# Kernel optimization log

Measured on AMD Instinct MI355X. Metric: run time of the kernel, lower is better.

The kernel has to match this reference:

```python
import jax, jax.numpy as jnp
import numpy as np

N = 1024        # nodes
E = 524288      # directed edges
FE_IN, FE = 2, 64   # edge feat in / mid
FC = 128        # candidate (node) feat
L = 3           # EGAT conv layers
NEG_SLOPE = 0.2 # DGL leaky_relu default


def setup_inputs() -> dict:
    key = jax.random.key(0)
    ks = jax.random.split(key, 12)
    s = 0.05
    return {
        "node_feature": jax.random.normal(ks[0], (N, FC), jnp.float32),
        "edge_feature": jax.random.normal(ks[1], (E, FE_IN), jnp.float32),
        "src": jax.random.randint(ks[2], (E,), 0, N, dtype=jnp.int32),
        "dst": jax.random.randint(ks[3], (E,), 0, N, dtype=jnp.int32),
        # input edge linear (bias=True)
        "W_in": jax.random.normal(ks[4], (FE_IN, FE), jnp.float32) * s,
        "b_in": jnp.zeros((FE,), jnp.float32),
        # per-layer EGATConv params (num_heads=1)
        "W_ni": jax.random.normal(ks[5], (L, FC, FE), jnp.float32) * s,
        "W_nj": jax.random.normal(ks[6], (L, FC, FE), jnp.float32) * s,
        "W_fij": jax.random.normal(ks[7], (L, FE, FE), jnp.float32) * s,
        "W_node": jax.random.normal(ks[8], (L, FC, FC), jnp.float32) * s,
        "attn": jax.random.normal(ks[9], (L, FE), jnp.float32) * s,
        "bias_node": jnp.zeros((L, FC), jnp.float32),
    }


def _edge_softmax(e, dst):
    # softmax of edge logits e[E] over incoming edges of each dst node
    m = jax.ops.segment_max(e, dst, num_segments=N)
    ex = jnp.exp(e - m[dst])
    z = jax.ops.segment_sum(ex, dst, num_segments=N)
    return ex / z[dst]


def reference(node_feature, edge_feature, src, dst, W_in, b_in,
              W_ni, W_nj, W_fij, W_node, attn, bias_node):
    node = node_feature                       # [N, FC]
    ef = edge_feature @ W_in + b_in           # [E, FE]
    for l in range(L):
        f_ni = node @ W_ni[l]                 # [N, FE]
        f_nj = node @ W_nj[l]                 # [N, FE]
        # edge messages: gather src/dst projections + edge projection
        f_out = jax.nn.leaky_relu(f_ni[src] + f_nj[dst] + ef @ W_fij[l],
                                  NEG_SLOPE)  # [E, FE]
        e = jnp.einsum('ef,f->e', f_out, attn[l])   # [E]
        a = _edge_softmax(e, dst)                    # [E]
        h = node @ W_node[l] + bias_node[l]          # [N, FC]
        new_node = jax.ops.segment_sum(a[:, None] * h[src], dst,
                                       num_segments=N)  # [N, FC]
        # residual fusion (use_residual=True, num_heads=1 so squeeze is a no-op)
        node = node + new_node
        ef = ef + f_out
    return node
```

## Files before the change

kernel.cpp:

```cpp
#include <hip/hip_runtime.h>

#define N_NODES 1024
#define E_EDGES 524288
#define FE 64
#define FC 128
#define NLAYERS 3

typedef unsigned short u16;
typedef unsigned int u32;
typedef __attribute__((ext_vector_type(8))) short bf16x8;
typedef __attribute__((ext_vector_type(4))) float f32x4;
typedef __attribute__((ext_vector_type(8))) unsigned short u16x8;
typedef __attribute__((ext_vector_type(4))) unsigned int u32x4;

__device__ __forceinline__ float bf2f(u16 u) {
    return __uint_as_float(((u32)u) << 16);
}
__device__ __forceinline__ u32 cvt2bf(float lo, float hi) {
    u32 r;
    asm("v_cvt_pk_bf16_f32 %0, %1, %2" : "=v"(r) : "v"(lo), "v"(hi));
    return r;
}
__device__ __forceinline__ u16 f2bf(float f) {
    return (u16)cvt2bf(f, 0.f);
}

__global__ __launch_bounds__(256) void setup_kernel(
    const float* __restrict__ node_feature, const float* __restrict__ Wfij,
    u16* __restrict__ Wt,
    const float* __restrict__ Wni, const float* __restrict__ Wnj,
    const float* __restrict__ Wnode, const float* __restrict__ bias,
    u16* __restrict__ fni, u16* __restrict__ fnj,
    float* __restrict__ h, float* __restrict__ S, float* __restrict__ nodeA)
{
    __shared__ float row[FC];
    const int d = blockIdx.x;
    const int t = threadIdx.x;

    reinterpret_cast<float4*>(S + (size_t)d * N_NODES)[t] = make_float4(0.f, 0.f, 0.f, 0.f);

    if (t < FC) {
        const float v = node_feature[d * FC + t];
        nodeA[d * FC + t] = v;
        row[t] = v;
    }
    if (d < (NLAYERS * FE * FE) / 256) {
        const int i = d * 256 + t;
        const int l = i >> 12, rem = i & 4095;
        const int n = rem >> 6, k = rem & 63;
        Wt[(u32)(l * 4096 + n * 64 + k)] = f2bf(Wfij[(u32)(l * 4096 + k * 64 + n)]);
    }
    __syncthreads();

    if (t < 64) {
        float a0 = 0.f, a1 = 0.f;
        #pragma unroll 8
        for (int k = 0; k < FC; k += 2) {
            a0 = fmaf(row[k],     Wni[k * FE + t], a0);
            a1 = fmaf(row[k + 1], Wni[(k + 1) * FE + t], a1);
        }
        fni[d * FE + t] = f2bf(a0 + a1);
    } else if (t < 128) {
        const int f = t - 64;
        float a0 = 0.f, a1 = 0.f;
        #pragma unroll 8
        for (int k = 0; k < FC; k += 2) {
            a0 = fmaf(row[k],     Wnj[k * FE + f], a0);
            a1 = fmaf(row[k + 1], Wnj[(k + 1) * FE + f], a1);
        }
        fnj[d * FE + f] = f2bf(a0 + a1);
    } else {
        const int c = t - 128;
        float a0 = bias[c], a1 = 0.f;
        #pragma unroll 8
        for (int k = 0; k < FC; k += 2) {
            a0 = fmaf(row[k],     Wnode[k * FC + c], a0);
            a1 = fmaf(row[k + 1], Wnode[(k + 1) * FC + c], a1);
        }
        h[d * FC + c] = a0 + a1;
    }
}

template <bool FIRST, bool WRITE_EF>
__global__ void edge_mfma_kernel(
    u16* __restrict__ ef,
    const float* __restrict__ x,
    const float* __restrict__ Win,
    const float* __restrict__ bin,
    const u16* __restrict__ Wt,
    const u16* __restrict__ fni, const u16* __restrict__ fnj,
    const int* __restrict__ src, const int* __restrict__ dst,
    const float* __restrict__ attn,
    float* __restrict__ S)
{
    __shared__ __align__(16) u16 stage[4][16][72];
    __shared__ __align__(16) u16 fol[WRITE_EF ? 4 : 1][16][72];

    const int lane = threadIdx.x & 63;
    const int wid  = threadIdx.x >> 6;
    const int l15  = lane & 15;
    const int grp  = lane >> 4;
    const int wbase = blockIdx.x * 64 + wid * 16;

    #pragma unroll
    for (int it = 0; it < 2; it++) {
        const int row = it * 8 + (lane >> 3);
        const int e = wbase + row;
        const int c8 = (lane & 7) * 8;
        const u16x8 a = *reinterpret_cast<const u16x8*>(fni + (u32)(src[e] * FE + c8));
        const u16x8 b = *reinterpret_cast<const u16x8*>(fnj + (u32)(dst[e] * FE + c8));
        u32x4 s;
        #pragma unroll
        for (int j = 0; j < 4; j++) {
            s[j] = cvt2bf(bf2f(a[2*j]) + bf2f(b[2*j]),
                          bf2f(a[2*j+1]) + bf2f(b[2*j+1]));
        }
        *reinterpret_cast<u32x4*>(&stage[wid][row][c8]) = s;
    }

    bf16x8 afr0, afr1;
    if constexpr (FIRST) {
        const float2 xx = *reinterpret_cast<const float2*>(x + 2 * (u32)(wbase + l15));
        #pragma unroll
        for (int half = 0; half < 2; half++) {
            const int c0 = half * 32 + grp * 8;
            const float4 wA0 = *reinterpret_cast<const float4*>(Win + c0);
            const float4 wA1 = *reinterpret_cast<const float4*>(Win + c0 + 4);
            const float4 wB0 = *reinterpret_cast<const float4*>(Win + FE + c0);
            const float4 wB1 = *reinterpret_cast<const float4*>(Win + FE + c0 + 4);
            const float4 b0  = *reinterpret_cast<const float4*>(bin + c0);
            const float4 b1  = *reinterpret_cast<const float4*>(bin + c0 + 4);
            u32x4 fr;
            fr[0] = cvt2bf(fmaf(xx.x, wA0.x, fmaf(xx.y, wB0.x, b0.x)),
                           fmaf(xx.x, wA0.y, fmaf(xx.y, wB0.y, b0.y)));
            fr[1] = cvt2bf(fmaf(xx.x, wA0.z, fmaf(xx.y, wB0.z, b0.z)),
                           fmaf(xx.x, wA0.w, fmaf(xx.y, wB0.w, b0.w)));
            fr[2] = cvt2bf(fmaf(xx.x, wA1.x, fmaf(xx.y, wB1.x, b1.x)),
                           fmaf(xx.x, wA1.y, fmaf(xx.y, wB1.y, b1.y)));
            fr[3] = cvt2bf(fmaf(xx.x, wA1.z, fmaf(xx.y, wB1.z, b1.z)),
                           fmaf(xx.x, wA1.w, fmaf(xx.y, wB1.w, b1.w)));
            if (half == 0) afr0 = (bf16x8)fr; else afr1 = (bf16x8)fr;
        }
    } else {
        const u32 arow = (u32)(wbase + l15) * FE;
        afr0 = *reinterpret_cast<const bf16x8*>(ef + arow + grp * 8);
        afr1 = *reinterpret_cast<const bf16x8*>(ef + arow + 32 + grp * 8);
    }

    bf16x8 bfr[2][4];
    #pragma unroll
    for (int ks = 0; ks < 2; ks++)
        #pragma unroll
        for (int nt = 0; nt < 4; nt++)
            bfr[ks][nt] = *reinterpret_cast<const bf16x8*>(
                Wt + (u32)((nt * 16 + l15) * 64 + ks * 32 + grp * 8));

    f32x4 acc[4];
    #pragma unroll
    for (int nt = 0; nt < 4; nt++) {
        acc[nt] = (f32x4){0.f, 0.f, 0.f, 0.f};
        acc[nt] = __builtin_amdgcn_mfma_f32_16x16x32_bf16(afr0, bfr[0][nt], acc[nt], 0, 0, 0);
        acc[nt] = __builtin_amdgcn_mfma_f32_16x16x32_bf16(afr1, bfr[1][nt], acc[nt], 0, 0, 0);
    }

    float an[4];
    #pragma unroll
    for (int nt = 0; nt < 4; nt++) an[nt] = attn[nt * 16 + l15] * 1.44269504088896f;

    __builtin_amdgcn_wave_barrier();

    float logit[4] = {0.f, 0.f, 0.f, 0.f};
    #pragma unroll
    for (int nt = 0; nt < 4; nt++) {
        const int n = nt * 16 + l15;
        #pragma unroll
        for (int r = 0; r < 4; r++) {
            const int row = grp * 4 + r;
            float v = acc[nt][r] + bf2f(stage[wid][row][n]);
            v = fmaxf(v, 0.2f * v);
            logit[r] = fmaf(v, an[nt], logit[r]);
            if constexpr (WRITE_EF) fol[wid][row][n] = f2bf(v);
        }
    }

    #pragma unroll
    for (int r = 0; r < 4; r++) {
        float t = logit[r];
        t += __shfl_xor(t, 1, 16);
        t += __shfl_xor(t, 2, 16);
        t += __shfl_xor(t, 4, 16);
        t += __shfl_xor(t, 8, 16);
        if (l15 == 0) {
            const int e = wbase + grp * 4 + r;
            atomicAdd(S + (u32)(dst[e] * N_NODES + src[e]), exp2f(t));
        }
    }

    if constexpr (WRITE_EF) {
        __builtin_amdgcn_wave_barrier();
        const u16x8 fo0 = *reinterpret_cast<const u16x8*>(&fol[wid][l15][grp * 8]);
        const u16x8 fo1 = *reinterpret_cast<const u16x8*>(&fol[wid][l15][32 + grp * 8]);
        u32x4 o0, o1;
        #pragma unroll
        for (int j = 0; j < 4; j++) {
            o0[j] = cvt2bf(bf2f((u16)afr0[2*j])   + bf2f(fo0[2*j]),
                           bf2f((u16)afr0[2*j+1]) + bf2f(fo0[2*j+1]));
            o1[j] = cvt2bf(bf2f((u16)afr1[2*j])   + bf2f(fo1[2*j]),
                           bf2f((u16)afr1[2*j+1]) + bf2f(fo1[2*j+1]));
        }
        u16* gp = ef + (u32)(wbase + l15) * FE;
        *reinterpret_cast<u32x4*>(gp + grp * 8) = o0;
        *reinterpret_cast<u32x4*>(gp + 32 + grp * 8) = o1;
    }
}

template <bool LAST>
__global__ __launch_bounds__(256) void spmm_kernel(
    float* __restrict__ S, const float* __restrict__ h,
    const float* __restrict__ nin, float* __restrict__ nout,
    const float* __restrict__ Wni, const float* __restrict__ Wnj,
    const float* __restrict__ Wnode, const float* __restrict__ bias,
    u16* __restrict__ fni, u16* __restrict__ fnj, float* __restrict__ hnext)
{
    __shared__ float red[256];
    __shared__ float rs[2];
    __shared__ float row[FC];
    const int d = blockIdx.x;
    const int t = threadIdx.x;
    const int c = t & 127;
    const int half = t >> 7;
    const float* Srow = S + (size_t)d * N_NODES + half * 512;
    const float* hp = h + (size_t)half * 512 * FC;
    float a0 = 0.f, a1 = 0.f, a2 = 0.f, a3 = 0.f;
    float r0 = 0.f, r1 = 0.f, r2 = 0.f, r3 = 0.f;
    #pragma unroll 4
    for (int n = 0; n < 512; n += 4) {
        const float s0 = Srow[n], s1 = Srow[n+1], s2 = Srow[n+2], s3 = Srow[n+3];
        r0 += s0; r1 += s1; r2 += s2; r3 += s3;
        a0 = fmaf(s0, hp[n * FC + c], a0);
        a1 = fmaf(s1, hp[(n+1) * FC + c], a1);
        a2 = fmaf(s2, hp[(n+2) * FC + c], a2);
        a3 = fmaf(s3, hp[(n+3) * FC + c], a3);
    }
    red[t] = (a0 + a1) + (a2 + a3);
    if (c == 0) rs[half] = (r0 + r1) + (r2 + r3);
    __syncthreads();

    if constexpr (!LAST) {
        reinterpret_cast<float4*>(S + (size_t)d * N_NODES)[t] = make_float4(0.f, 0.f, 0.f, 0.f);
    }
    if (half == 0) {
        const float v = nin[d * FC + c] + (red[c] + red[128 + c]) / (rs[0] + rs[1]);
        nout[d * FC + c] = v;
        if constexpr (!LAST) row[c] = v;
    }

    if constexpr (!LAST) {
        __syncthreads();
        if (t < 64) {
            float b0 = 0.f, b1 = 0.f;
            #pragma unroll 8
            for (int k = 0; k < FC; k += 2) {
                b0 = fmaf(row[k],     Wni[k * FE + t], b0);
                b1 = fmaf(row[k + 1], Wni[(k + 1) * FE + t], b1);
            }
            fni[d * FE + t] = f2bf(b0 + b1);
        } else if (t < 128) {
            const int f = t - 64;
            float b0 = 0.f, b1 = 0.f;
            #pragma unroll 8
            for (int k = 0; k < FC; k += 2) {
                b0 = fmaf(row[k],     Wnj[k * FE + f], b0);
                b1 = fmaf(row[k + 1], Wnj[(k + 1) * FE + f], b1);
            }
            fnj[d * FE + f] = f2bf(b0 + b1);
        } else {
            const int cc = t - 128;
            float b0 = bias[cc], b1 = 0.f;
            #pragma unroll 8
            for (int k = 0; k < FC; k += 2) {
                b0 = fmaf(row[k],     Wnode[k * FC + cc], b0);
                b1 = fmaf(row[k + 1], Wnode[(k + 1) * FC + cc], b1);
            }
            hnext[d * FC + cc] = b0 + b1;
        }
    }
}

extern "C" void kernel_launch(void* const* d_in, const int* in_sizes, int n_in,
                              void* d_out, int out_size, void* d_ws, size_t ws_size,
                              hipStream_t stream)
{
    const float* node_feature = (const float*)d_in[0];
    const float* edge_feature = (const float*)d_in[1];
    const int*   src          = (const int*)d_in[2];
    const int*   dst          = (const int*)d_in[3];
    const float* W_in         = (const float*)d_in[4];
    const float* b_in         = (const float*)d_in[5];
    const float* W_ni         = (const float*)d_in[6];
    const float* W_nj         = (const float*)d_in[7];
    const float* W_fij        = (const float*)d_in[8];
    const float* W_node       = (const float*)d_in[9];
    const float* attn         = (const float*)d_in[10];
    const float* bias_node    = (const float*)d_in[11];
    float* out = (float*)d_out;

    char* ws = (char*)d_ws;
    size_t off = 0;
    auto alloc = [&](size_t bytes) -> void* {
        void* pp = ws + off;
        off += (bytes + 255) & ~(size_t)255;
        return pp;
    };
    u16*   ef    = (u16*)alloc((size_t)E_EDGES * FE * sizeof(u16));
    u16*   fni   = (u16*)alloc(N_NODES * FE * sizeof(u16));
    u16*   fnj   = (u16*)alloc(N_NODES * FE * sizeof(u16));
    float* h0    = (float*)alloc(N_NODES * FC * sizeof(float));
    float* h1    = (float*)alloc(N_NODES * FC * sizeof(float));
    float* S     = (float*)alloc((size_t)N_NODES * N_NODES * sizeof(float));
    float* nodeA = (float*)alloc(N_NODES * FC * sizeof(float));
    u16*   Wt    = (u16*)alloc((size_t)NLAYERS * FE * FE * sizeof(u16));
    float* hbuf[2] = {h0, h1};

    setup_kernel<<<N_NODES, 256, 0, stream>>>(
        node_feature, W_fij, Wt, W_ni, W_nj, W_node, bias_node,
        fni, fnj, h0, S, nodeA);

    for (int l = 0; l < NLAYERS; l++) {
        float* hl = hbuf[l & 1];
        float* hn = hbuf[(l + 1) & 1];

        if (l == 0) {
            edge_mfma_kernel<true, true><<<E_EDGES / 64, 256, 0, stream>>>(
                ef, edge_feature, W_in, b_in, Wt + (size_t)l * FE * FE,
                fni, fnj, src, dst, attn + (size_t)l * FE, S);
        } else if (l == NLAYERS - 1) {
            edge_mfma_kernel<false, false><<<E_EDGES / 64, 256, 0, stream>>>(
                ef, nullptr, nullptr, nullptr, Wt + (size_t)l * FE * FE,
                fni, fnj, src, dst, attn + (size_t)l * FE, S);
        } else {
            edge_mfma_kernel<false, true><<<E_EDGES / 64, 256, 0, stream>>>(
                ef, nullptr, nullptr, nullptr, Wt + (size_t)l * FE * FE,
                fni, fnj, src, dst, attn + (size_t)l * FE, S);
        }

        if (l == NLAYERS - 1) {
            spmm_kernel<true><<<N_NODES, 256, 0, stream>>>(
                S, hl, nodeA, out,
                nullptr, nullptr, nullptr, nullptr, nullptr, nullptr, nullptr);
        } else {
            const int ln = l + 1;
            spmm_kernel<false><<<N_NODES, 256, 0, stream>>>(
                S, hl, nodeA, nodeA,
                W_ni + (size_t)ln * FC * FE, W_nj + (size_t)ln * FC * FE,
                W_node + (size_t)ln * FC * FC, bias_node + (size_t)ln * FC,
                fni, fnj, hn);
        }
    }
}
```

Measured before the change: 280.0 us.

## Process two edge tiles per wave and four destination rows per spmm block

The edge kernel now handles 128 edges per block, with each wave doing two 16-edge tiles. All src/dst indices and fni/fnj gathers are issued up front, and indices are broadcast with shuffles instead of reloaded. The spmm kernel computes four destination rows per block, so each h load is reused across four S rows, and the row sums come from a separate vectorized pass. The aim is more memory-level parallelism and less redundant h traffic, at the cost of higher register pressure and fewer blocks.

```diff
diff --git a/kernel.cpp b/kernel.cpp
--- a/kernel.cpp
+++ b/kernel.cpp
@@ -100,51 +100,60 @@
     const int wid  = threadIdx.x >> 6;
     const int l15  = lane & 15;
     const int grp  = lane >> 4;
-    const int wbase = blockIdx.x * 64 + wid * 16;
-
-    #pragma unroll
-    for (int it = 0; it < 2; it++) {
-        const int row = it * 8 + (lane >> 3);
-        const int e = wbase + row;
-        const int c8 = (lane & 7) * 8;
-        const u16x8 a = *reinterpret_cast<const u16x8*>(fni + (u32)(src[e] * FE + c8));
-        const u16x8 b = *reinterpret_cast<const u16x8*>(fnj + (u32)(dst[e] * FE + c8));
-        u32x4 s;
-        #pragma unroll
-        for (int j = 0; j < 4; j++) {
-            s[j] = cvt2bf(bf2f(a[2*j]) + bf2f(b[2*j]),
-                          bf2f(a[2*j+1]) + bf2f(b[2*j+1]));
-        }
-        *reinterpret_cast<u32x4*>(&stage[wid][row][c8]) = s;
-    }
-
-    bf16x8 afr0, afr1;
-    if constexpr (FIRST) {
-        const float2 xx = *reinterpret_cast<const float2*>(x + 2 * (u32)(wbase + l15));
-        #pragma unroll
-        for (int half = 0; half < 2; half++) {
-            const int c0 = half * 32 + grp * 8;
-            const float4 wA0 = *reinterpret_cast<const float4*>(Win + c0);
-            const float4 wA1 = *reinterpret_cast<const float4*>(Win + c0 + 4);
-            const float4 wB0 = *reinterpret_cast<const float4*>(Win + FE + c0);
-            const float4 wB1 = *reinterpret_cast<const float4*>(Win + FE + c0 + 4);
-            const float4 b0  = *reinterpret_cast<const float4*>(bin + c0);
-            const float4 b1  = *reinterpret_cast<const float4*>(bin + c0 + 4);
-            u32x4 fr;
-            fr[0] = cvt2bf(fmaf(xx.x, wA0.x, fmaf(xx.y, wB0.x, b0.x)),
-                           fmaf(xx.x, wA0.y, fmaf(xx.y, wB0.y, b0.y)));
-            fr[1] = cvt2bf(fmaf(xx.x, wA0.z, fmaf(xx.y, wB0.z, b0.z)),
-                           fmaf(xx.x, wA0.w, fmaf(xx.y, wB0.w, b0.w)));
-            fr[2] = cvt2bf(fmaf(xx.x, wA1.x, fmaf(xx.y, wB1.x, b1.x)),
-                           fmaf(xx.x, wA1.y, fmaf(xx.y, wB1.y, b1.y)));
-            fr[3] = cvt2bf(fmaf(xx.x, wA1.z, fmaf(xx.y, wB1.z, b1.z)),
-                           fmaf(xx.x, wA1.w, fmaf(xx.y, wB1.w, b1.w)));
-            if (half == 0) afr0 = (bf16x8)fr; else afr1 = (bf16x8)fr;
-        }
-    } else {
-        const u32 arow = (u32)(wbase + l15) * FE;
-        afr0 = *reinterpret_cast<const bf16x8*>(ef + arow + grp * 8);
-        afr1 = *reinterpret_cast<const bf16x8*>(ef + arow + 32 + grp * 8);
+    const int block0 = blockIdx.x * 128;
+
+    int tb[2], sv[2], dv[2];
+    #pragma unroll
+    for (int tt = 0; tt < 2; tt++) {
+        tb[tt] = block0 + tt * 64 + wid * 16;
+        sv[tt] = src[tb[tt] + l15];
+        dv[tt] = dst[tb[tt] + l15];
+    }
+
+    u16x8 ga[2][2], gb[2][2];
+    #pragma unroll
+    for (int tt = 0; tt < 2; tt++) {
+        #pragma unroll
+        for (int it = 0; it < 2; it++) {
+            const int row = it * 8 + (lane >> 3);
+            const int c8 = (lane & 7) * 8;
+            const int s = __shfl(sv[tt], row, 16);
+            const int d = __shfl(dv[tt], row, 16);
+            ga[tt][it] = *reinterpret_cast<const u16x8*>(fni + (u32)(s * FE + c8));
+            gb[tt][it] = *reinterpret_cast<const u16x8*>(fnj + (u32)(d * FE + c8));
+        }
+    }
+
+    bf16x8 afr[2][2];
+    #pragma unroll
+    for (int tt = 0; tt < 2; tt++) {
+        if constexpr (FIRST) {
+            const float2 xx = *reinterpret_cast<const float2*>(x + 2 * (u32)(tb[tt] + l15));
+            #pragma unroll
+            for (int half = 0; half < 2; half++) {
+                const int c0 = half * 32 + grp * 8;
+                const float4 wA0 = *reinterpret_cast<const float4*>(Win + c0);
+                const float4 wA1 = *reinterpret_cast<const float4*>(Win + c0 + 4);
+                const float4 wB0 = *reinterpret_cast<const float4*>(Win + FE + c0);
+                const float4 wB1 = *reinterpret_cast<const float4*>(Win + FE + c0 + 4);
+                const float4 b0  = *reinterpret_cast<const float4*>(bin + c0);
+                const float4 b1  = *reinterpret_cast<const float4*>(bin + c0 + 4);
+                u32x4 fr;
+                fr[0] = cvt2bf(fmaf(xx.x, wA0.x, fmaf(xx.y, wB0.x, b0.x)),
+                               fmaf(xx.x, wA0.y, fmaf(xx.y, wB0.y, b0.y)));
+                fr[1] = cvt2bf(fmaf(xx.x, wA0.z, fmaf(xx.y, wB0.z, b0.z)),
+                               fmaf(xx.x, wA0.w, fmaf(xx.y, wB0.w, b0.w)));
+                fr[2] = cvt2bf(fmaf(xx.x, wA1.x, fmaf(xx.y, wB1.x, b1.x)),
+                               fmaf(xx.x, wA1.y, fmaf(xx.y, wB1.y, b1.y)));
+                fr[3] = cvt2bf(fmaf(xx.x, wA1.z, fmaf(xx.y, wB1.z, b1.z)),
+                               fmaf(xx.x, wA1.w, fmaf(xx.y, wB1.w, b1.w)));
+                afr[tt][half] = (bf16x8)fr;
+            }
+        } else {
+            const u32 arow = (u32)(tb[tt] + l15) * FE;
+            afr[tt][0] = *reinterpret_cast<const bf16x8*>(ef + arow + grp * 8);
+            afr[tt][1] = *reinterpret_cast<const bf16x8*>(ef + arow + 32 + grp * 8);
+        }
     }
 
     bf16x8 bfr[2][4];
@@ -155,62 +164,81 @@
             bfr[ks][nt] = *reinterpret_cast<const bf16x8*>(
                 Wt + (u32)((nt * 16 + l15) * 64 + ks * 32 + grp * 8));
 
-    f32x4 acc[4];
-    #pragma unroll
-    for (int nt = 0; nt < 4; nt++) {
-        acc[nt] = (f32x4){0.f, 0.f, 0.f, 0.f};
-        acc[nt] = __builtin_amdgcn_mfma_f32_16x16x32_bf16(afr0, bfr[0][nt], acc[nt], 0, 0, 0);
-        acc[nt] = __builtin_amdgcn_mfma_f32_16x16x32_bf16(afr1, bfr[1][nt], acc[nt], 0, 0, 0);
-    }
-
     float an[4];
     #pragma unroll
     for (int nt = 0; nt < 4; nt++) an[nt] = attn[nt * 16 + l15] * 1.44269504088896f;
 
-    __builtin_amdgcn_wave_barrier();
-
-    float logit[4] = {0.f, 0.f, 0.f, 0.f};
-    #pragma unroll
-    for (int nt = 0; nt < 4; nt++) {
-        const int n = nt * 16 + l15;
+    #pragma unroll
+    for (int tt = 0; tt < 2; tt++) {
+        #pragma unroll
+        for (int it = 0; it < 2; it++) {
+            const int row = it * 8 + (lane >> 3);
+            const int c8 = (lane & 7) * 8;
+            u32x4 s;
+            #pragma unroll
+            for (int j = 0; j < 4; j++) {
+                s[j] = cvt2bf(bf2f(ga[tt][it][2*j])   + bf2f(gb[tt][it][2*j]),
+                              bf2f(ga[tt][it][2*j+1]) + bf2f(gb[tt][it][2*j+1]));
+            }
+            *reinterpret_cast<u32x4*>(&stage[wid][row][c8]) = s;
+        }
+
+        f32x4 acc[4];
+        #pragma unroll
+        for (int nt = 0; nt < 4; nt++) {
+            acc[nt] = (f32x4){0.f, 0.f, 0.f, 0.f};
+            acc[nt] = __builtin_amdgcn_mfma_f32_16x16x32_bf16(afr[tt][0], bfr[0][nt], acc[nt], 0, 0, 0);
+            acc[nt] = __builtin_amdgcn_mfma_f32_16x16x32_bf16(afr[tt][1], bfr[1][nt], acc[nt], 0, 0, 0);
+        }
+
+        __builtin_amdgcn_wave_barrier();
+
+        float logit[4] = {0.f, 0.f, 0.f, 0.f};
+        #pragma unroll
+        for (int nt = 0; nt < 4; nt++) {
+            const int n = nt * 16 + l15;
+            #pragma unroll
+            for (int r = 0; r < 4; r++) {
+                const int row = grp * 4 + r;
+                float v = acc[nt][r] + bf2f(stage[wid][row][n]);
+                v = fmaxf(v, 0.2f * v);
+                logit[r] = fmaf(v, an[nt], logit[r]);
+                if constexpr (WRITE_EF) fol[wid][row][n] = f2bf(v);
+            }
+        }
+
         #pragma unroll
         for (int r = 0; r < 4; r++) {
-            const int row = grp * 4 + r;
-            float v = acc[nt][r] + bf2f(stage[wid][row][n]);
-            v = fmaxf(v, 0.2f * v);
-            logit[r] = fmaf(v, an[nt], logit[r]);
-            if constexpr (WRITE_EF) fol[wid][row][n] = f2bf(v);
-        }
-    }
-
-    #pragma unroll
-    for (int r = 0; r < 4; r++) {
-        float t = logit[r];
-        t += __shfl_xor(t, 1, 16);
-        t += __shfl_xor(t, 2, 16);
-        t += __shfl_xor(t, 4, 16);
-        t += __shfl_xor(t, 8, 16);
-        if (l15 == 0) {
-            const int e = wbase + grp * 4 + r;
-            atomicAdd(S + (u32)(dst[e] * N_NODES + src[e]), exp2f(t));
-        }
-    }
-
-    if constexpr (WRITE_EF) {
+            float t = logit[r];
+            t += __shfl_xor(t, 1, 16);
+            t += __shfl_xor(t, 2, 16);
+            t += __shfl_xor(t, 4, 16);
+            t += __shfl_xor(t, 8, 16);
+            const int sidx = __shfl(sv[tt], grp * 4 + r, 16);
+            const int didx = __shfl(dv[tt], grp * 4 + r, 16);
+            if (l15 == 0) {
+                atomicAdd(S + (u32)(didx * N_NODES + sidx), exp2f(t));
+            }
+        }
+
+        if constexpr (WRITE_EF) {
+            __builtin_amdgcn_wave_barrier();
+            const u16x8 fo0 = *reinterpret_cast<const u16x8*>(&fol[wid][l15][grp * 8]);
+            const u16x8 fo1 = *reinterpret_cast<const u16x8*>(&fol[wid][l15][32 + grp * 8]);
+            u32x4 o0, o1;
+            #pragma unroll
+            for (int j = 0; j < 4; j++) {
+                o0[j] = cvt2bf(bf2f((u16)afr[tt][0][2*j])   + bf2f(fo0[2*j]),
+                               bf2f((u16)afr[tt][0][2*j+1]) + bf2f(fo0[2*j+1]));
+                o1[j] = cvt2bf(bf2f((u16)afr[tt][1][2*j])   + bf2f(fo1[2*j]),
+                               bf2f((u16)afr[tt][1][2*j+1]) + bf2f(fo1[2*j+1]));
+            }
+            u16* gp = ef + (u32)(tb[tt] + l15) * FE;
+            *reinterpret_cast<u32x4*>(gp + grp * 8) = o0;
+            *reinterpret_cast<u32x4*>(gp + 32 + grp * 8) = o1;
+        }
+
         __builtin_amdgcn_wave_barrier();
-        const u16x8 fo0 = *reinterpret_cast<const u16x8*>(&fol[wid][l15][grp * 8]);
-        const u16x8 fo1 = *reinterpret_cast<const u16x8*>(&fol[wid][l15][32 + grp * 8]);
-        u32x4 o0, o1;
-        #pragma unroll
-        for (int j = 0; j < 4; j++) {
-            o0[j] = cvt2bf(bf2f((u16)afr0[2*j])   + bf2f(fo0[2*j]),
-                           bf2f((u16)afr0[2*j+1]) + bf2f(fo0[2*j+1]));
-            o1[j] = cvt2bf(bf2f((u16)afr1[2*j])   + bf2f(fo1[2*j]),
-                           bf2f((u16)afr1[2*j+1]) + bf2f(fo1[2*j+1]));
-        }
-        u16* gp = ef + (u32)(wbase + l15) * FE;
-        *reinterpret_cast<u32x4*>(gp + grp * 8) = o0;
-        *reinterpret_cast<u32x4*>(gp + 32 + grp * 8) = o1;
     }
 }
 
@@ -222,67 +250,100 @@
     const float* __restrict__ Wnode, const float* __restrict__ bias,
     u16* __restrict__ fni, u16* __restrict__ fnj, float* __restrict__ hnext)
 {
-    __shared__ float red[256];
-    __shared__ float rs[2];
-    __shared__ float row[FC];
-    const int d = blockIdx.x;
+    __shared__ float red[2][128][4];
+    __shared__ float rs[4];
+    __shared__ float row[4][FC];
+    const int d0 = blockIdx.x * 4;
     const int t = threadIdx.x;
     const int c = t & 127;
     const int half = t >> 7;
-    const float* Srow = S + (size_t)d * N_NODES + half * 512;
-    const float* hp = h + (size_t)half * 512 * FC;
+
+    const float* hp = h + (u32)(half * 512 * FC) + c;
+    const u32 sbase = (u32)(d0 * N_NODES) + half * 512;
     float a0 = 0.f, a1 = 0.f, a2 = 0.f, a3 = 0.f;
-    float r0 = 0.f, r1 = 0.f, r2 = 0.f, r3 = 0.f;
     #pragma unroll 4
-    for (int n = 0; n < 512; n += 4) {
-        const float s0 = Srow[n], s1 = Srow[n+1], s2 = Srow[n+2], s3 = Srow[n+3];
-        r0 += s0; r1 += s1; r2 += s2; r3 += s3;
-        a0 = fmaf(s0, hp[n * FC + c], a0);
-        a1 = fmaf(s1, hp[(n+1) * FC + c], a1);
-        a2 = fmaf(s2, hp[(n+2) * FC + c], a2);
-        a3 = fmaf(s3, hp[(n+3) * FC + c], a3);
-    }
-    red[t] = (a0 + a1) + (a2 + a3);
-    if (c == 0) rs[half] = (r0 + r1) + (r2 + r3);
+    for (int n = 0; n < 512; n++) {
+        const float hv = hp[(u32)n * FC];
+        const float s0 = S[sbase + n];
+        const float s1 = S[sbase + N_NODES + n];
+        const float s2 = S[sbase + 2 * N_NODES + n];
+        const float s3 = S[sbase + 3 * N_NODES + n];
+        a0 = fmaf(s0, hv, a0);
+        a1 = fmaf(s1, hv, a1);
+        a2 = fmaf(s2, hv, a2);
+        a3 = fmaf(s3, hv, a3);
+    }
+    red[half][c][0] = a0; red[half][c][1] = a1;
+    red[half][c][2] = a2; red[half][c][3] = a3;
+
+    {
+        const int w = t >> 6, wl = t & 63;
+        const float4* sr = reinterpret_cast<const float4*>(S + (u32)(d0 + w) * N_NODES);
+        float rsv = 0.f;
+        #pragma unroll
+        for (int q = 0; q < 4; q++) {
+            const float4 v = sr[wl + 64 * q];
+            rsv += (v.x + v.y) + (v.z + v.w);
+        }
+        rsv += __shfl_xor(rsv, 1);  rsv += __shfl_xor(rsv, 2);
+        rsv += __shfl_xor(rsv, 4);  rsv += __shfl_xor(rsv, 8);
+        rsv += __shfl_xor(rsv, 16); rsv += __shfl_xor(rsv, 32);
+        if (wl == 0) rs[w] = rsv;
+    }
     __syncthreads();
 
     if constexpr (!LAST) {
-        reinterpret_cast<float4*>(S + (size_t)d * N_NODES)[t] = make_float4(0.f, 0.f, 0.f, 0.f);
-    }
-    if (half == 0) {
-        const float v = nin[d * FC + c] + (red[c] + red[128 + c]) / (rs[0] + rs[1]);
-        nout[d * FC + c] = v;
-        if constexpr (!LAST) row[c] = v;
+        float4* sz = reinterpret_cast<float4*>(S + (u32)d0 * N_NODES);
+        #pragma unroll
+        for (int q = 0; q < 4; q++) sz[t + 256 * q] = make_float4(0.f, 0.f, 0.f, 0.f);
+    }
+    if (t < 128) {
+        #pragma unroll
+        for (int r = 0; r < 4; r++) {
+            const float v = nin[(u32)(d0 + r) * FC + t]
+                          + (red[0][t][r] + red[1][t][r]) / rs[r];
+            nout[(u32)(d0 + r) * FC + t] = v;
+            if constexpr (!LAST) row[r][t] = v;
+        }
     }
 
     if constexpr (!LAST) {
         __syncthreads();
         if (t < 64) {
-            float b0 = 0.f, b1 = 0.f;
-            #pragma unroll 8
-            for (int k = 0; k < FC; k += 2) {
-                b0 = fmaf(row[k],     Wni[k * FE + t], b0);
-                b1 = fmaf(row[k + 1], Wni[(k + 1) * FE + t], b1);
-            }
-            fni[d * FE + t] = f2bf(b0 + b1);
+            #pragma unroll
+            for (int r = 0; r < 4; r++) {
+                float b0 = 0.f, b1 = 0.f;
+                #pragma unroll 8
+                for (int k = 0; k < FC; k += 2) {
+                    b0 = fmaf(row[r][k],     Wni[k * FE + t], b0);
+                    b1 = fmaf(row[r][k + 1], Wni[(k + 1) * FE + t], b1);
+                }
+                fni[(u32)(d0 + r) * FE + t] = f2bf(b0 + b1);
+            }
         } else if (t < 128) {
             const int f = t - 64;
-            float b0 = 0.f, b1 = 0.f;
-            #pragma unroll 8
-            for (int k = 0; k < FC; k += 2) {
-                b0 = fmaf(row[k],     Wnj[k * FE + f], b0);
-                b1 = fmaf(row[k + 1], Wnj[(k + 1) * FE + f], b1);
-            }
-            fnj[d * FE + f] = f2bf(b0 + b1);
+            #pragma unroll
+            for (int r = 0; r < 4; r++) {
+                float b0 = 0.f, b1 = 0.f;
+                #pragma unroll 8
+                for (int k = 0; k < FC; k += 2) {
+                    b0 = fmaf(row[r][k],     Wnj[k * FE + f], b0);
+                    b1 = fmaf(row[r][k + 1], Wnj[(k + 1) * FE + f], b1);
+                }
+                fnj[(u32)(d0 + r) * FE + f] = f2bf(b0 + b1);
+            }
         } else {
             const int cc = t - 128;
-            float b0 = bias[cc], b1 = 0.f;
-            #pragma unroll 8
-            for (int k = 0; k < FC; k += 2) {
-                b0 = fmaf(row[k],     Wnode[k * FC + cc], b0);
-                b1 = fmaf(row[k + 1], Wnode[(k + 1) * FC + cc], b1);
-            }
-            hnext[d * FC + cc] = b0 + b1;
+            #pragma unroll
+            for (int r = 0; r < 4; r++) {
+                float b0 = bias[cc], b1 = 0.f;
+                #pragma unroll 8
+                for (int k = 0; k < FC; k += 2) {
+                    b0 = fmaf(row[r][k],     Wnode[k * FC + cc], b0);
+                    b1 = fmaf(row[r][k + 1], Wnode[(k + 1) * FC + cc], b1);
+                }
+                hnext[(u32)(d0 + r) * FC + cc] = b0 + b1;
+            }
         }
     }
 }
@@ -331,26 +392,26 @@
         float* hn = hbuf[(l + 1) & 1];
 
         if (l == 0) {
-            edge_mfma_kernel<true, true><<<E_EDGES / 64, 256, 0, stream>>>(
+            edge_mfma_kernel<true, true><<<E_EDGES / 128, 256, 0, stream>>>(
                 ef, edge_feature, W_in, b_in, Wt + (size_t)l * FE * FE,
                 fni, fnj, src, dst, attn + (size_t)l * FE, S);
         } else if (l == NLAYERS - 1) {
-            edge_mfma_kernel<false, false><<<E_EDGES / 64, 256, 0, stream>>>(
+            edge_mfma_kernel<false, false><<<E_EDGES / 128, 256, 0, stream>>>(
                 ef, nullptr, nullptr, nullptr, Wt + (size_t)l * FE * FE,
                 fni, fnj, src, dst, attn + (size_t)l * FE, S);
         } else {
-            edge_mfma_kernel<false, true><<<E_EDGES / 64, 256, 0, stream>>>(
+            edge_mfma_kernel<false, true><<<E_EDGES / 128, 256, 0, stream>>>(
                 ef, nullptr, nullptr, nullptr, Wt + (size_t)l * FE * FE,
                 fni, fnj, src, dst, attn + (size_t)l * FE, S);
         }
 
         if (l == NLAYERS - 1) {
-            spmm_kernel<true><<<N_NODES, 256, 0, stream>>>(
+            spmm_kernel<true><<<N_NODES / 4, 256, 0, stream>>>(
                 S, hl, nodeA, out,
                 nullptr, nullptr, nullptr, nullptr, nullptr, nullptr, nullptr);
         } else {
             const int ln = l + 1;
-            spmm_kernel<false><<<N_NODES, 256, 0, stream>>>(
+            spmm_kernel<false><<<N_NODES / 4, 256, 0, stream>>>(
                 S, hl, nodeA, nodeA,
                 W_ni + (size_t)ln * FC * FE, W_nj + (size_t)ln * FC * FE,
                 W_node + (size_t)ln * FC * FC, bias_node + (size_t)ln * FC,
```

New measurement: 272.1 us. 2.8% less time.

## Process two edge tiles per wave with early batched gathers and shuffled indices

Applied to the files above, without the earlier changes.

Each wave now handles two 16-edge tiles per block, halving the grid. It loads src/dst once per lane and broadcasts them with shuffles instead of re-reading them. All fni/fnj gathers and ef loads for both tiles are issued up front, so more memory requests are in flight before the MFMA and epilogue work. This also amortizes the weight-fragment and attention loads over twice as many edges, at the cost of higher register pressure and fewer blocks. Some 64-bit index math in the spmm kernel is narrowed to 32-bit.

```diff
diff --git a/kernel.cpp b/kernel.cpp
--- a/kernel.cpp
+++ b/kernel.cpp
@@ -100,51 +100,60 @@
     const int wid  = threadIdx.x >> 6;
     const int l15  = lane & 15;
     const int grp  = lane >> 4;
-    const int wbase = blockIdx.x * 64 + wid * 16;
-
-    #pragma unroll
-    for (int it = 0; it < 2; it++) {
-        const int row = it * 8 + (lane >> 3);
-        const int e = wbase + row;
-        const int c8 = (lane & 7) * 8;
-        const u16x8 a = *reinterpret_cast<const u16x8*>(fni + (u32)(src[e] * FE + c8));
-        const u16x8 b = *reinterpret_cast<const u16x8*>(fnj + (u32)(dst[e] * FE + c8));
-        u32x4 s;
-        #pragma unroll
-        for (int j = 0; j < 4; j++) {
-            s[j] = cvt2bf(bf2f(a[2*j]) + bf2f(b[2*j]),
-                          bf2f(a[2*j+1]) + bf2f(b[2*j+1]));
-        }
-        *reinterpret_cast<u32x4*>(&stage[wid][row][c8]) = s;
-    }
-
-    bf16x8 afr0, afr1;
-    if constexpr (FIRST) {
-        const float2 xx = *reinterpret_cast<const float2*>(x + 2 * (u32)(wbase + l15));
-        #pragma unroll
-        for (int half = 0; half < 2; half++) {
-            const int c0 = half * 32 + grp * 8;
-            const float4 wA0 = *reinterpret_cast<const float4*>(Win + c0);
-            const float4 wA1 = *reinterpret_cast<const float4*>(Win + c0 + 4);
-            const float4 wB0 = *reinterpret_cast<const float4*>(Win + FE + c0);
-            const float4 wB1 = *reinterpret_cast<const float4*>(Win + FE + c0 + 4);
-            const float4 b0  = *reinterpret_cast<const float4*>(bin + c0);
-            const float4 b1  = *reinterpret_cast<const float4*>(bin + c0 + 4);
-            u32x4 fr;
-            fr[0] = cvt2bf(fmaf(xx.x, wA0.x, fmaf(xx.y, wB0.x, b0.x)),
-                           fmaf(xx.x, wA0.y, fmaf(xx.y, wB0.y, b0.y)));
-            fr[1] = cvt2bf(fmaf(xx.x, wA0.z, fmaf(xx.y, wB0.z, b0.z)),
-                           fmaf(xx.x, wA0.w, fmaf(xx.y, wB0.w, b0.w)));
-            fr[2] = cvt2bf(fmaf(xx.x, wA1.x, fmaf(xx.y, wB1.x, b1.x)),
-                           fmaf(xx.x, wA1.y, fmaf(xx.y, wB1.y, b1.y)));
-            fr[3] = cvt2bf(fmaf(xx.x, wA1.z, fmaf(xx.y, wB1.z, b1.z)),
-                           fmaf(xx.x, wA1.w, fmaf(xx.y, wB1.w, b1.w)));
-            if (half == 0) afr0 = (bf16x8)fr; else afr1 = (bf16x8)fr;
-        }
-    } else {
-        const u32 arow = (u32)(wbase + l15) * FE;
-        afr0 = *reinterpret_cast<const bf16x8*>(ef + arow + grp * 8);
-        afr1 = *reinterpret_cast<const bf16x8*>(ef + arow + 32 + grp * 8);
+    const int block0 = blockIdx.x * 128;
+
+    int tb[2], sv[2], dv[2];
+    #pragma unroll
+    for (int tt = 0; tt < 2; tt++) {
+        tb[tt] = block0 + tt * 64 + wid * 16;
+        sv[tt] = src[tb[tt] + l15];
+        dv[tt] = dst[tb[tt] + l15];
+    }
+
+    u16x8 ga[2][2], gb[2][2];
+    #pragma unroll
+    for (int tt = 0; tt < 2; tt++) {
+        #pragma unroll
+        for (int it = 0; it < 2; it++) {
+            const int row = it * 8 + (lane >> 3);
+            const int c8 = (lane & 7) * 8;
+            const int s = __shfl(sv[tt], row, 16);
+            const int d = __shfl(dv[tt], row, 16);
+            ga[tt][it] = *reinterpret_cast<const u16x8*>(fni + (u32)(s * FE + c8));
+            gb[tt][it] = *reinterpret_cast<const u16x8*>(fnj + (u32)(d * FE + c8));
+        }
+    }
+
+    bf16x8 afr[2][2];
+    #pragma unroll
+    for (int tt = 0; tt < 2; tt++) {
+        if constexpr (FIRST) {
+            const float2 xx = *reinterpret_cast<const float2*>(x + 2 * (u32)(tb[tt] + l15));
+            #pragma unroll
+            for (int half = 0; half < 2; half++) {
+                const int c0 = half * 32 + grp * 8;
+                const float4 wA0 = *reinterpret_cast<const float4*>(Win + c0);
+                const float4 wA1 = *reinterpret_cast<const float4*>(Win + c0 + 4);
+                const float4 wB0 = *reinterpret_cast<const float4*>(Win + FE + c0);
+                const float4 wB1 = *reinterpret_cast<const float4*>(Win + FE + c0 + 4);
+                const float4 b0  = *reinterpret_cast<const float4*>(bin + c0);
+                const float4 b1  = *reinterpret_cast<const float4*>(bin + c0 + 4);
+                u32x4 fr;
+                fr[0] = cvt2bf(fmaf(xx.x, wA0.x, fmaf(xx.y, wB0.x, b0.x)),
+                               fmaf(xx.x, wA0.y, fmaf(xx.y, wB0.y, b0.y)));
+                fr[1] = cvt2bf(fmaf(xx.x, wA0.z, fmaf(xx.y, wB0.z, b0.z)),
+                               fmaf(xx.x, wA0.w, fmaf(xx.y, wB0.w, b0.w)));
+                fr[2] = cvt2bf(fmaf(xx.x, wA1.x, fmaf(xx.y, wB1.x, b1.x)),
+                               fmaf(xx.x, wA1.y, fmaf(xx.y, wB1.y, b1.y)));
+                fr[3] = cvt2bf(fmaf(xx.x, wA1.z, fmaf(xx.y, wB1.z, b1.z)),
+                               fmaf(xx.x, wA1.w, fmaf(xx.y, wB1.w, b1.w)));
+                afr[tt][half] = (bf16x8)fr;
+            }
+        } else {
+            const u32 arow = (u32)(tb[tt] + l15) * FE;
+            afr[tt][0] = *reinterpret_cast<const bf16x8*>(ef + arow + grp * 8);
+            afr[tt][1] = *reinterpret_cast<const bf16x8*>(ef + arow + 32 + grp * 8);
+        }
     }
 
     bf16x8 bfr[2][4];
@@ -155,62 +164,81 @@
             bfr[ks][nt] = *reinterpret_cast<const bf16x8*>(
                 Wt + (u32)((nt * 16 + l15) * 64 + ks * 32 + grp * 8));
 
-    f32x4 acc[4];
-    #pragma unroll
-    for (int nt = 0; nt < 4; nt++) {
-        acc[nt] = (f32x4){0.f, 0.f, 0.f, 0.f};
-        acc[nt] = __builtin_amdgcn_mfma_f32_16x16x32_bf16(afr0, bfr[0][nt], acc[nt], 0, 0, 0);
-        acc[nt] = __builtin_amdgcn_mfma_f32_16x16x32_bf16(afr1, bfr[1][nt], acc[nt], 0, 0, 0);
-    }
-
     float an[4];
     #pragma unroll
     for (int nt = 0; nt < 4; nt++) an[nt] = attn[nt * 16 + l15] * 1.44269504088896f;
 
-    __builtin_amdgcn_wave_barrier();
-
-    float logit[4] = {0.f, 0.f, 0.f, 0.f};
-    #pragma unroll
-    for (int nt = 0; nt < 4; nt++) {
-        const int n = nt * 16 + l15;
+    #pragma unroll
+    for (int tt = 0; tt < 2; tt++) {
+        #pragma unroll
+        for (int it = 0; it < 2; it++) {
+            const int row = it * 8 + (lane >> 3);
+            const int c8 = (lane & 7) * 8;
+            u32x4 s;
+            #pragma unroll
+            for (int j = 0; j < 4; j++) {
+                s[j] = cvt2bf(bf2f(ga[tt][it][2*j])   + bf2f(gb[tt][it][2*j]),
+                              bf2f(ga[tt][it][2*j+1]) + bf2f(gb[tt][it][2*j+1]));
+            }
+            *reinterpret_cast<u32x4*>(&stage[wid][row][c8]) = s;
+        }
+
+        f32x4 acc[4];
+        #pragma unroll
+        for (int nt = 0; nt < 4; nt++) {
+            acc[nt] = (f32x4){0.f, 0.f, 0.f, 0.f};
+            acc[nt] = __builtin_amdgcn_mfma_f32_16x16x32_bf16(afr[tt][0], bfr[0][nt], acc[nt], 0, 0, 0);
+            acc[nt] = __builtin_amdgcn_mfma_f32_16x16x32_bf16(afr[tt][1], bfr[1][nt], acc[nt], 0, 0, 0);
+        }
+
+        __builtin_amdgcn_wave_barrier();
+
+        float logit[4] = {0.f, 0.f, 0.f, 0.f};
+        #pragma unroll
+        for (int nt = 0; nt < 4; nt++) {
+            const int n = nt * 16 + l15;
+            #pragma unroll
+            for (int r = 0; r < 4; r++) {
+                const int row = grp * 4 + r;
+                float v = acc[nt][r] + bf2f(stage[wid][row][n]);
+                v = fmaxf(v, 0.2f * v);
+                logit[r] = fmaf(v, an[nt], logit[r]);
+                if constexpr (WRITE_EF) fol[wid][row][n] = f2bf(v);
+            }
+        }
+
         #pragma unroll
         for (int r = 0; r < 4; r++) {
-            const int row = grp * 4 + r;
-            float v = acc[nt][r] + bf2f(stage[wid][row][n]);
-            v = fmaxf(v, 0.2f * v);
-            logit[r] = fmaf(v, an[nt], logit[r]);
-            if constexpr (WRITE_EF) fol[wid][row][n] = f2bf(v);
-        }
-    }
-
-    #pragma unroll
-    for (int r = 0; r < 4; r++) {
-        float t = logit[r];
-        t += __shfl_xor(t, 1, 16);
-        t += __shfl_xor(t, 2, 16);
-        t += __shfl_xor(t, 4, 16);
-        t += __shfl_xor(t, 8, 16);
-        if (l15 == 0) {
-            const int e = wbase + grp * 4 + r;
-            atomicAdd(S + (u32)(dst[e] * N_NODES + src[e]), exp2f(t));
-        }
-    }
-
-    if constexpr (WRITE_EF) {
+            float t = logit[r];
+            t += __shfl_xor(t, 1, 16);
+            t += __shfl_xor(t, 2, 16);
+            t += __shfl_xor(t, 4, 16);
+            t += __shfl_xor(t, 8, 16);
+            const int sidx = __shfl(sv[tt], grp * 4 + r, 16);
+            const int didx = __shfl(dv[tt], grp * 4 + r, 16);
+            if (l15 == 0) {
+                atomicAdd(S + (u32)(didx * N_NODES + sidx), exp2f(t));
+            }
+        }
+
+        if constexpr (WRITE_EF) {
+            __builtin_amdgcn_wave_barrier();
+            const u16x8 fo0 = *reinterpret_cast<const u16x8*>(&fol[wid][l15][grp * 8]);
+            const u16x8 fo1 = *reinterpret_cast<const u16x8*>(&fol[wid][l15][32 + grp * 8]);
+            u32x4 o0, o1;
+            #pragma unroll
+            for (int j = 0; j < 4; j++) {
+                o0[j] = cvt2bf(bf2f((u16)afr[tt][0][2*j])   + bf2f(fo0[2*j]),
+                               bf2f((u16)afr[tt][0][2*j+1]) + bf2f(fo0[2*j+1]));
+                o1[j] = cvt2bf(bf2f((u16)afr[tt][1][2*j])   + bf2f(fo1[2*j]),
+                               bf2f((u16)afr[tt][1][2*j+1]) + bf2f(fo1[2*j+1]));
+            }
+            u16* gp = ef + (u32)(tb[tt] + l15) * FE;
+            *reinterpret_cast<u32x4*>(gp + grp * 8) = o0;
+            *reinterpret_cast<u32x4*>(gp + 32 + grp * 8) = o1;
+        }
+
         __builtin_amdgcn_wave_barrier();
-        const u16x8 fo0 = *reinterpret_cast<const u16x8*>(&fol[wid][l15][grp * 8]);
-        const u16x8 fo1 = *reinterpret_cast<const u16x8*>(&fol[wid][l15][32 + grp * 8]);
-        u32x4 o0, o1;
-        #pragma unroll
-        for (int j = 0; j < 4; j++) {
-            o0[j] = cvt2bf(bf2f((u16)afr0[2*j])   + bf2f(fo0[2*j]),
-                           bf2f((u16)afr0[2*j+1]) + bf2f(fo0[2*j+1]));
-            o1[j] = cvt2bf(bf2f((u16)afr1[2*j])   + bf2f(fo1[2*j]),
-                           bf2f((u16)afr1[2*j+1]) + bf2f(fo1[2*j+1]));
-        }
-        u16* gp = ef + (u32)(wbase + l15) * FE;
-        *reinterpret_cast<u32x4*>(gp + grp * 8) = o0;
-        *reinterpret_cast<u32x4*>(gp + 32 + grp * 8) = o1;
     }
 }
 
@@ -229,8 +257,8 @@
     const int t = threadIdx.x;
     const int c = t & 127;
     const int half = t >> 7;
-    const float* Srow = S + (size_t)d * N_NODES + half * 512;
-    const float* hp = h + (size_t)half * 512 * FC;
+    const float* Srow = S + (u32)d * N_NODES + half * 512;
+    const float* hp = h + (u32)(half * 512 * FC);
     float a0 = 0.f, a1 = 0.f, a2 = 0.f, a3 = 0.f;
     float r0 = 0.f, r1 = 0.f, r2 = 0.f, r3 = 0.f;
     #pragma unroll 4
@@ -247,7 +275,7 @@
     __syncthreads();
 
     if constexpr (!LAST) {
-        reinterpret_cast<float4*>(S + (size_t)d * N_NODES)[t] = make_float4(0.f, 0.f, 0.f, 0.f);
+        reinterpret_cast<float4*>(S + (u32)d * N_NODES)[t] = make_float4(0.f, 0.f, 0.f, 0.f);
     }
     if (half == 0) {
         const float v = nin[d * FC + c] + (red[c] + red[128 + c]) / (rs[0] + rs[1]);
@@ -331,15 +359,15 @@
         float* hn = hbuf[(l + 1) & 1];
 
         if (l == 0) {
-            edge_mfma_kernel<true, true><<<E_EDGES / 64, 256, 0, stream>>>(
+            edge_mfma_kernel<true, true><<<E_EDGES / 128, 256, 0, stream>>>(
                 ef, edge_feature, W_in, b_in, Wt + (size_t)l * FE * FE,
                 fni, fnj, src, dst, attn + (size_t)l * FE, S);
         } else if (l == NLAYERS - 1) {
-            edge_mfma_kernel<false, false><<<E_EDGES / 64, 256, 0, stream>>>(
+            edge_mfma_kernel<false, false><<<E_EDGES / 128, 256, 0, stream>>>(
                 ef, nullptr, nullptr, nullptr, Wt + (size_t)l * FE * FE,
                 fni, fnj, src, dst, attn + (size_t)l * FE, S);
         } else {
-            edge_mfma_kernel<false, true><<<E_EDGES / 64, 256, 0, stream>>>(
+            edge_mfma_kernel<false, true><<<E_EDGES / 128, 256, 0, stream>>>(
                 ef, nullptr, nullptr, nullptr, Wt + (size_t)l * FE * FE,
                 fni, fnj, src, dst, attn + (size_t)l * FE, S);
         }
```

After: 233.6 us. 1.2x faster.
